# Kernel tuning notes

Hardware: AMD Instinct MI355X
Metric: run time of the kernel (lower is better)

## Reference

```python
import jax, jax.numpy as jnp
import numpy as np

DIM_V = 1024
NUM_HEADS = 64            # per the module arg name; actually the per-chunk size
DIM_SPLIT = DIM_V // NUM_HEADS  # 16 = effective number of attention heads (module quirk)
N_Q, N_K = 2048, 2048
DIM_Q, DIM_K = 1024, 1024


def setup_inputs() -> dict:
    key = jax.random.key(0)
    ks = jax.random.split(key, 10)
    s = 0.02
    return {
        "Q": jax.random.normal(ks[0], (N_Q, DIM_Q), dtype=jnp.float32),
        "K": jax.random.normal(ks[1], (N_K, DIM_K), dtype=jnp.float32),
        "Wq": jax.random.normal(ks[2], (DIM_V, DIM_Q), dtype=jnp.float32) * s,
        "bq": jax.random.normal(ks[3], (DIM_V,), dtype=jnp.float32) * s,
        "Wk": jax.random.normal(ks[4], (DIM_V, DIM_K), dtype=jnp.float32) * s,
        "bk": jax.random.normal(ks[5], (DIM_V,), dtype=jnp.float32) * s,
        "Wv": jax.random.normal(ks[6], (DIM_V, DIM_K), dtype=jnp.float32) * s,
        "bv": jax.random.normal(ks[7], (DIM_V,), dtype=jnp.float32) * s,
        "Wo": jax.random.normal(ks[8], (DIM_V, DIM_V), dtype=jnp.float32) * s,
        "bo": jax.random.normal(ks[9], (DIM_V,), dtype=jnp.float32) * s,
    }


def _split_heads(x):
    # jnp.split(x[None], DIM_SPLIT, axis=2) then concat on axis 0 ==
    # [DIM_SPLIT, n, NUM_HEADS] with chunk h = x[:, h*NUM_HEADS:(h+1)*NUM_HEADS]
    n = x.shape[0]
    return x.reshape(n, DIM_SPLIT, NUM_HEADS).transpose(1, 0, 2)


def reference(Q, K, Wq, bq, Wk, bk, Wv, bv, Wo, bo):
    q = Q @ Wq.T + bq            # [n_q, dim_V]
    k = K @ Wk.T + bk            # [n_k, dim_V]
    v = K @ Wv.T + bv            # [n_k, dim_V]
    Q_ = _split_heads(q)         # [H, n_q, d] with H=DIM_SPLIT, d=NUM_HEADS
    K_ = _split_heads(k)
    V_ = _split_heads(v)
    # Faithful to source: softmax first, THEN divide by sqrt(dim_V)
    A = jax.nn.softmax(jnp.einsum('hqd,hkd->hqk', Q_, K_), axis=-1)
    A = A / jnp.sqrt(jnp.float32(DIM_V))
    O = (Q_ + jnp.einsum('hqk,hkd->hqd', A, V_)).reshape(-1, DIM_V)  # [n_q, dim_V]
    # res1 = identity (ln=False)
    O = O + jax.nn.relu(O @ Wo.T + bo)
    # res2 = identity (ln=False)
    return O
```

## Files before the change

kernel.cpp:

```cpp
#include <hip/hip_runtime.h>
#include <cstdint>

typedef unsigned short u16;
typedef __attribute__((ext_vector_type(8))) short short8;
typedef __attribute__((ext_vector_type(4))) float f32x4;

__device__ __forceinline__ u16 f2b(float f) {
  uint32_t u = __float_as_uint(f);
  u += 0x7fffu + ((u >> 16) & 1u);
  return (u16)(u >> 16);
}
__device__ __forceinline__ float b2f(u16 b) {
  return __uint_as_float(((uint32_t)b) << 16);
}

__global__ __launch_bounds__(256) void cast_all(
    const float* __restrict__ Q, const float* __restrict__ K,
    const float* __restrict__ Wq, const float* __restrict__ Wk,
    const float* __restrict__ Wv, const float* __restrict__ Wo,
    u16* __restrict__ xq, u16* __restrict__ xk,
    u16* __restrict__ wq, u16* __restrict__ wk,
    u16* __restrict__ wv, u16* __restrict__ wo) {
  int g = blockIdx.x * 256 + threadIdx.x;
  const float* src; u16* dst; int off;
  if      (g <  524288) { src = Q;  dst = xq; off = g; }
  else if (g < 1048576) { src = K;  dst = xk; off = g -  524288; }
  else if (g < 1310720) { src = Wq; dst = wq; off = g - 1048576; }
  else if (g < 1572864) { src = Wk; dst = wk; off = g - 1310720; }
  else if (g < 1835008) { src = Wv; dst = wv; off = g - 1572864; }
  else                  { src = Wo; dst = wo; off = g - 1835008; }
  float4 v = reinterpret_cast<const float4*>(src)[off];
  ushort4 o4;
  o4.x = f2b(v.x); o4.y = f2b(v.y); o4.z = f2b(v.z); o4.w = f2b(v.w);
  reinterpret_cast<ushort4*>(dst)[off] = o4;
}

__global__ __launch_bounds__(256) void gemm3(
    const u16* __restrict__ xq, const u16* __restrict__ xk,
    const u16* __restrict__ wq, const u16* __restrict__ wk,
    const u16* __restrict__ wv,
    const float* __restrict__ bq, const float* __restrict__ bk,
    const float* __restrict__ bv,
    u16* __restrict__ qb, u16* __restrict__ kb, u16* __restrict__ vT) {
  __shared__ __align__(16) u16 sA[64 * 40];
  __shared__ __align__(16) u16 sB[64 * 40];
  const int t = threadIdx.x, blk = blockIdx.x, z = blockIdx.y;
  const u16 *A, *B; const float* bias; u16* C; int ldC, mbase, nbase; bool brow;
  if (z == 0)      { A = xq; B = wq; bias = bq; C = qb; ldC = 1024;
                     mbase = (blk >> 4) * 64; nbase = (blk & 15) * 64; brow = false; }
  else if (z == 1) { A = xk; B = wk; bias = bk; C = kb; ldC = 1024;
                     mbase = (blk >> 4) * 64; nbase = (blk & 15) * 64; brow = false; }
  else             { A = wv; B = xk; bias = bv; C = vT; ldC = 2048;
                     mbase = (blk >> 5) * 64; nbase = (blk & 31) * 64; brow = true; }
  const int lane = t & 63, wid = t >> 6;
  const int wy = wid >> 1, wx = wid & 1;
  const int m = lane & 15, quad = lane >> 4;
  const int srow = t >> 2, scb = (t & 3) * 8;
  const u16* gA = A + (mbase + srow) * 1024 + scb;
  const u16* gB = B + (nbase + srow) * 1024 + scb;
  uint4 ra = *(const uint4*)gA;
  uint4 rb = *(const uint4*)gB;

  f32x4 acc[2][2];
#pragma unroll
  for (int i = 0; i < 2; i++)
#pragma unroll
    for (int j = 0; j < 2; j++) acc[i][j] = (f32x4){0.f, 0.f, 0.f, 0.f};

  for (int kb_ = 0; kb_ < 32; ++kb_) {
    __syncthreads();
    *(uint4*)(&sA[srow * 40 + scb]) = ra;
    *(uint4*)(&sB[srow * 40 + scb]) = rb;
    if (kb_ < 31) {
      ra = *(const uint4*)(gA + (kb_ + 1) * 32);
      rb = *(const uint4*)(gB + (kb_ + 1) * 32);
    }
    __syncthreads();
    short8 af[2], bf[2];
#pragma unroll
    for (int mi = 0; mi < 2; mi++)
      af[mi] = *(const short8*)(&sA[(wy * 32 + mi * 16 + m) * 40 + quad * 8]);
#pragma unroll
    for (int ni = 0; ni < 2; ni++)
      bf[ni] = *(const short8*)(&sB[(wx * 32 + ni * 16 + m) * 40 + quad * 8]);
#pragma unroll
    for (int mi = 0; mi < 2; mi++)
#pragma unroll
      for (int ni = 0; ni < 2; ni++)
        acc[mi][ni] = __builtin_amdgcn_mfma_f32_16x16x32_bf16(
            af[mi], bf[ni], acc[mi][ni], 0, 0, 0);
  }

#pragma unroll
  for (int mi = 0; mi < 2; mi++)
#pragma unroll
    for (int ni = 0; ni < 2; ni++) {
      const int col = nbase + wx * 32 + ni * 16 + m;
      const float bcol = brow ? 0.f : bias[col];
#pragma unroll
      for (int r = 0; r < 4; r++) {
        const int row = mbase + wy * 32 + mi * 16 + quad * 4 + r;
        const float bval = brow ? bias[row] : bcol;
        C[row * ldC + col] = f2b(acc[mi][ni][r] + bval);
      }
    }
}

__global__ __launch_bounds__(256) void gemm_out(
    const u16* __restrict__ A, const u16* __restrict__ B,
    const float* __restrict__ bias, const u16* __restrict__ Res,
    float* __restrict__ out) {
  __shared__ __align__(16) u16 sA[64 * 40];
  __shared__ __align__(16) u16 sB[64 * 40];
  const int t = threadIdx.x, blk = blockIdx.x;
  const int mbase = (blk >> 4) * 64, nbase = (blk & 15) * 64;
  const int lane = t & 63, wid = t >> 6;
  const int wy = wid >> 1, wx = wid & 1;
  const int m = lane & 15, quad = lane >> 4;
  const int srow = t >> 2, scb = (t & 3) * 8;
  const u16* gA = A + (mbase + srow) * 1024 + scb;
  const u16* gB = B + (nbase + srow) * 1024 + scb;
  uint4 ra = *(const uint4*)gA;
  uint4 rb = *(const uint4*)gB;

  f32x4 acc[2][2];
#pragma unroll
  for (int i = 0; i < 2; i++)
#pragma unroll
    for (int j = 0; j < 2; j++) acc[i][j] = (f32x4){0.f, 0.f, 0.f, 0.f};

  for (int kb_ = 0; kb_ < 32; ++kb_) {
    __syncthreads();
    *(uint4*)(&sA[srow * 40 + scb]) = ra;
    *(uint4*)(&sB[srow * 40 + scb]) = rb;
    if (kb_ < 31) {
      ra = *(const uint4*)(gA + (kb_ + 1) * 32);
      rb = *(const uint4*)(gB + (kb_ + 1) * 32);
    }
    __syncthreads();
    short8 af[2], bf[2];
#pragma unroll
    for (int mi = 0; mi < 2; mi++)
      af[mi] = *(const short8*)(&sA[(wy * 32 + mi * 16 + m) * 40 + quad * 8]);
#pragma unroll
    for (int ni = 0; ni < 2; ni++)
      bf[ni] = *(const short8*)(&sB[(wx * 32 + ni * 16 + m) * 40 + quad * 8]);
#pragma unroll
    for (int mi = 0; mi < 2; mi++)
#pragma unroll
      for (int ni = 0; ni < 2; ni++)
        acc[mi][ni] = __builtin_amdgcn_mfma_f32_16x16x32_bf16(
            af[mi], bf[ni], acc[mi][ni], 0, 0, 0);
  }

#pragma unroll
  for (int mi = 0; mi < 2; mi++)
#pragma unroll
    for (int ni = 0; ni < 2; ni++) {
      const int col = nbase + wx * 32 + ni * 16 + m;
      const float bcol = bias[col];
#pragma unroll
      for (int r = 0; r < 4; r++) {
        const int row = mbase + wy * 32 + mi * 16 + quad * 4 + r;
        out[row * 1024 + col] =
            b2f(Res[row * 1024 + col]) + fmaxf(acc[mi][ni][r] + bcol, 0.f);
      }
    }
}

__global__ __launch_bounds__(256) void flash(
    const u16* __restrict__ q, const u16* __restrict__ k,
    const u16* __restrict__ vT, u16* __restrict__ po, float* __restrict__ lp) {
  __shared__ __align__(16) u16 sK[64 * 72];
  __shared__ __align__(16) u16 sV[64 * 72];
  __shared__ __align__(16) u16 sP[4 * 32 * 72];
  const int t = threadIdx.x;
  const int qt = blockIdx.x, h = blockIdx.y, sp = blockIdx.z;
  const int lane = t & 63, wid = t >> 6;
  const int m = lane & 15, quad = lane >> 4;
  const int colbase = h * 64;
  const int pbase = wid * 2304;
  const int kbase = sp * 1024;

  short8 aq[2][2];
#pragma unroll
  for (int mi = 0; mi < 2; mi++)
#pragma unroll
    for (int g = 0; g < 2; g++)
      aq[mi][g] = *(const short8*)(
          &q[(qt * 128 + wid * 32 + mi * 16 + m) * 1024 + colbase + g * 32 + quad * 8]);

  f32x4 o[2][4];
  float lpart[2][4];
#pragma unroll
  for (int mi = 0; mi < 2; mi++)
#pragma unroll
    for (int nt = 0; nt < 4; nt++) o[mi][nt] = (f32x4){0.f, 0.f, 0.f, 0.f};
#pragma unroll
  for (int mi = 0; mi < 2; mi++)
#pragma unroll
    for (int r = 0; r < 4; r++) lpart[mi][r] = 0.f;

  const int srow = t >> 2, scb = (t & 3) * 16;
  const u16* gK = k + (kbase + srow) * 1024 + colbase + scb;
  const u16* gV = vT + (colbase + srow) * 2048 + kbase + scb;

  uint4 rk0 = *(const uint4*)(gK), rk1 = *(const uint4*)(gK + 8);
  uint4 rv0 = *(const uint4*)(gV), rv1 = *(const uint4*)(gV + 8);

  for (int kt = 0; kt < 16; ++kt) {
    __syncthreads();
    *(uint4*)(&sK[srow * 72 + scb])     = rk0;
    *(uint4*)(&sK[srow * 72 + scb + 8]) = rk1;
    *(uint4*)(&sV[srow * 72 + scb])     = rv0;
    *(uint4*)(&sV[srow * 72 + scb + 8]) = rv1;
    if (kt < 15) {
      rk0 = *(const uint4*)(gK + (kt + 1) * 65536);
      rk1 = *(const uint4*)(gK + (kt + 1) * 65536 + 8);
      rv0 = *(const uint4*)(gV + (kt + 1) * 64);
      rv1 = *(const uint4*)(gV + (kt + 1) * 64 + 8);
    }
    __syncthreads();

    f32x4 s[2][4];
#pragma unroll
    for (int nt = 0; nt < 4; nt++) {
      short8 bk0 = *(const short8*)(&sK[(nt * 16 + m) * 72 + quad * 8]);
      short8 bk1 = *(const short8*)(&sK[(nt * 16 + m) * 72 + 32 + quad * 8]);
#pragma unroll
      for (int mi = 0; mi < 2; mi++) {
        f32x4 a = (f32x4){0.f, 0.f, 0.f, 0.f};
        a = __builtin_amdgcn_mfma_f32_16x16x32_bf16(aq[mi][0], bk0, a, 0, 0, 0);
        a = __builtin_amdgcn_mfma_f32_16x16x32_bf16(aq[mi][1], bk1, a, 0, 0, 0);
        s[mi][nt] = a;
      }
    }

#pragma unroll
    for (int mi = 0; mi < 2; mi++)
#pragma unroll
      for (int nt = 0; nt < 4; nt++)
#pragma unroll
        for (int r = 0; r < 4; r++) {
          const float p = __expf(s[mi][nt][r] - 16.0f);
          lpart[mi][r] += p;
          sP[pbase + (mi * 16 + quad * 4 + r) * 72 + nt * 16 + m] = f2b(p);
        }

    short8 pa[2][2];
#pragma unroll
    for (int mi = 0; mi < 2; mi++)
#pragma unroll
      for (int g = 0; g < 2; g++)
        pa[mi][g] = *(const short8*)(&sP[pbase + (mi * 16 + m) * 72 + g * 32 + quad * 8]);
#pragma unroll
    for (int nt = 0; nt < 4; nt++) {
      short8 bv0 = *(const short8*)(&sV[(nt * 16 + m) * 72 + quad * 8]);
      short8 bv1 = *(const short8*)(&sV[(nt * 16 + m) * 72 + 32 + quad * 8]);
#pragma unroll
      for (int mi = 0; mi < 2; mi++) {
        o[mi][nt] = __builtin_amdgcn_mfma_f32_16x16x32_bf16(pa[mi][0], bv0, o[mi][nt], 0, 0, 0);
        o[mi][nt] = __builtin_amdgcn_mfma_f32_16x16x32_bf16(pa[mi][1], bv1, o[mi][nt], 0, 0, 0);
      }
    }
  }

#pragma unroll
  for (int mi = 0; mi < 2; mi++)
#pragma unroll
    for (int r = 0; r < 4; r++) {
#pragma unroll
      for (int off = 1; off < 16; off <<= 1)
        lpart[mi][r] += __shfl_xor(lpart[mi][r], off);
    }

#pragma unroll
  for (int mi = 0; mi < 2; mi++)
#pragma unroll
    for (int r = 0; r < 4; r++) {
      const int qg = qt * 128 + wid * 32 + mi * 16 + quad * 4 + r;
      const int base = ((sp * 16 + h) * 2048 + qg) * 64;
#pragma unroll
      for (int nt = 0; nt < 4; nt++)
        po[base + nt * 16 + m] = f2b(o[mi][nt][r]);
      if (m == 0) lp[(sp * 16 + h) * 2048 + qg] = lpart[mi][r];
    }
}

__global__ __launch_bounds__(256) void combine(
    const u16* __restrict__ po, const float* __restrict__ lp,
    const u16* __restrict__ qb, u16* __restrict__ ob) {
  const int idx = blockIdx.x * 256 + threadIdx.x;
  const int dq = idx & 15, qg = (idx >> 4) & 2047, h = idx >> 15;
  float acc0 = 0.f, acc1 = 0.f, acc2 = 0.f, acc3 = 0.f, l = 0.f;
#pragma unroll
  for (int s = 0; s < 2; s++) {
    const ushort4 p4 = *(const ushort4*)&po[(((s * 16 + h) * 2048 + qg) * 64) + dq * 4];
    acc0 += b2f(p4.x); acc1 += b2f(p4.y); acc2 += b2f(p4.z); acc3 += b2f(p4.w);
    l += lp[(s * 16 + h) * 2048 + qg];
  }
  const float inv = 1.0f / (l * 32.0f);
  const ushort4 q4 = *(const ushort4*)&qb[qg * 1024 + h * 64 + dq * 4];
  ushort4 o4;
  o4.x = f2b(b2f(q4.x) + acc0 * inv);
  o4.y = f2b(b2f(q4.y) + acc1 * inv);
  o4.z = f2b(b2f(q4.z) + acc2 * inv);
  o4.w = f2b(b2f(q4.w) + acc3 * inv);
  *(ushort4*)&ob[(h * 128 + (qg >> 4)) * 1024 + (qg & 15) * 64 + dq * 4] = o4;
}

extern "C" void kernel_launch(void* const* d_in, const int* in_sizes, int n_in,
                              void* d_out, int out_size, void* d_ws, size_t ws_size,
                              hipStream_t stream) {
  const float* Q  = (const float*)d_in[0];
  const float* K  = (const float*)d_in[1];
  const float* Wq = (const float*)d_in[2];
  const float* bq = (const float*)d_in[3];
  const float* Wk = (const float*)d_in[4];
  const float* bk = (const float*)d_in[5];
  const float* Wv = (const float*)d_in[6];
  const float* bv = (const float*)d_in[7];
  const float* Wo = (const float*)d_in[8];
  const float* bo = (const float*)d_in[9];
  float* out = (float*)d_out;

  u16* ws = (u16*)d_ws;
  u16* xq  = ws;
  u16* xk  = xq  + 2097152;
  u16* wqb = xk  + 2097152;
  u16* wkb = wqb + 1048576;
  u16* wvb = wkb + 1048576;
  u16* wob = wvb + 1048576;
  u16* qb  = wob + 1048576;
  u16* kb  = qb  + 2097152;
  u16* vT  = kb  + 2097152;
  u16* ob  = vT  + 2097152;
  u16*   po = ws;
  float* lp = (float*)(ws + 4194304);

  cast_all<<<8192, 256, 0, stream>>>(Q, K, Wq, Wk, Wv, Wo, xq, xk, wqb, wkb, wvb, wob);

  gemm3<<<dim3(512, 3), 256, 0, stream>>>(xq, xk, wqb, wkb, wvb, bq, bk, bv, qb, kb, vT);

  flash<<<dim3(16, 16, 2), 256, 0, stream>>>(qb, kb, vT, po, lp);

  combine<<<2048, 256, 0, stream>>>(po, lp, qb, ob);

  gemm_out<<<512, 256, 0, stream>>>(ob, wob, bo, ob, out);
}
```

Measured before the change: 176.7 us.

## Enlarge gemm3 M tile, split flash keys 4-way, transpose QK^T MFMA for packed P stores

The projection GEMM now uses 128x64 tiles with four M fragments per wave, which halves the block count and raises B-tile reuse. The flash kernel splits the key range into four chunks instead of two, giving more blocks for parallelism. It also swaps the MFMA operands so each lane holds a row of S, which lets P be stored as packed bf16 pairs and shortens the row-sum reduction to two shuffles. The combine kernel now reads four partials, and the partial buffers move to a separate workspace region, at the cost of more partial-output traffic.

```diff
diff --git a/kernel.cpp b/kernel.cpp
--- a/kernel.cpp
+++ b/kernel.cpp
@@ -1,4 +1,5 @@
 #include <hip/hip_runtime.h>
+#include <hip/hip_bf16.h>
 #include <cstdint>
 
 typedef unsigned short u16;
@@ -12,6 +13,10 @@
 }
 __device__ __forceinline__ float b2f(u16 b) {
   return __uint_as_float(((uint32_t)b) << 16);
+}
+__device__ __forceinline__ uint32_t pk2bf(float a, float b) {
+  __hip_bfloat162 t = __float22bfloat162_rn(make_float2(a, b));
+  return *(uint32_t*)&t;
 }
 
 __global__ __launch_bounds__(256) void cast_all(
@@ -42,49 +47,55 @@
     const float* __restrict__ bq, const float* __restrict__ bk,
     const float* __restrict__ bv,
     u16* __restrict__ qb, u16* __restrict__ kb, u16* __restrict__ vT) {
-  __shared__ __align__(16) u16 sA[64 * 40];
+  __shared__ __align__(16) u16 sA[128 * 40];
   __shared__ __align__(16) u16 sB[64 * 40];
   const int t = threadIdx.x, blk = blockIdx.x, z = blockIdx.y;
   const u16 *A, *B; const float* bias; u16* C; int ldC, mbase, nbase; bool brow;
   if (z == 0)      { A = xq; B = wq; bias = bq; C = qb; ldC = 1024;
-                     mbase = (blk >> 4) * 64; nbase = (blk & 15) * 64; brow = false; }
+                     mbase = (blk >> 4) * 128; nbase = (blk & 15) * 64; brow = false; }
   else if (z == 1) { A = xk; B = wk; bias = bk; C = kb; ldC = 1024;
-                     mbase = (blk >> 4) * 64; nbase = (blk & 15) * 64; brow = false; }
+                     mbase = (blk >> 4) * 128; nbase = (blk & 15) * 64; brow = false; }
   else             { A = wv; B = xk; bias = bv; C = vT; ldC = 2048;
-                     mbase = (blk >> 5) * 64; nbase = (blk & 31) * 64; brow = true; }
+                     mbase = (blk >> 5) * 128; nbase = (blk & 31) * 64; brow = true; }
   const int lane = t & 63, wid = t >> 6;
   const int wy = wid >> 1, wx = wid & 1;
   const int m = lane & 15, quad = lane >> 4;
-  const int srow = t >> 2, scb = (t & 3) * 8;
-  const u16* gA = A + (mbase + srow) * 1024 + scb;
-  const u16* gB = B + (nbase + srow) * 1024 + scb;
-  uint4 ra = *(const uint4*)gA;
-  uint4 rb = *(const uint4*)gB;
-
-  f32x4 acc[2][2];
-#pragma unroll
-  for (int i = 0; i < 2; i++)
+
+  const int arow = t >> 1, acb = (t & 1) * 16;
+  const int brow_ = t >> 2, bcb = (t & 3) * 8;
+  const u16* gA = A + (mbase + arow) * 1024 + acb;
+  const u16* gB = B + (nbase + brow_) * 1024 + bcb;
+
+  uint4 ra0 = *(const uint4*)(gA);
+  uint4 ra1 = *(const uint4*)(gA + 8);
+  uint4 rb0 = *(const uint4*)(gB);
+
+  f32x4 acc[4][2];
+#pragma unroll
+  for (int i = 0; i < 4; i++)
 #pragma unroll
     for (int j = 0; j < 2; j++) acc[i][j] = (f32x4){0.f, 0.f, 0.f, 0.f};
 
   for (int kb_ = 0; kb_ < 32; ++kb_) {
     __syncthreads();
-    *(uint4*)(&sA[srow * 40 + scb]) = ra;
-    *(uint4*)(&sB[srow * 40 + scb]) = rb;
+    *(uint4*)(&sA[arow * 40 + acb])     = ra0;
+    *(uint4*)(&sA[arow * 40 + acb + 8]) = ra1;
+    *(uint4*)(&sB[brow_ * 40 + bcb])    = rb0;
     if (kb_ < 31) {
-      ra = *(const uint4*)(gA + (kb_ + 1) * 32);
-      rb = *(const uint4*)(gB + (kb_ + 1) * 32);
-    }
-    __syncthreads();
-    short8 af[2], bf[2];
-#pragma unroll
-    for (int mi = 0; mi < 2; mi++)
-      af[mi] = *(const short8*)(&sA[(wy * 32 + mi * 16 + m) * 40 + quad * 8]);
+      ra0 = *(const uint4*)(gA + (kb_ + 1) * 32);
+      ra1 = *(const uint4*)(gA + (kb_ + 1) * 32 + 8);
+      rb0 = *(const uint4*)(gB + (kb_ + 1) * 32);
+    }
+    __syncthreads();
+    short8 af[4], bf[2];
+#pragma unroll
+    for (int mi = 0; mi < 4; mi++)
+      af[mi] = *(const short8*)(&sA[(wy * 64 + mi * 16 + m) * 40 + quad * 8]);
 #pragma unroll
     for (int ni = 0; ni < 2; ni++)
       bf[ni] = *(const short8*)(&sB[(wx * 32 + ni * 16 + m) * 40 + quad * 8]);
 #pragma unroll
-    for (int mi = 0; mi < 2; mi++)
+    for (int mi = 0; mi < 4; mi++)
 #pragma unroll
       for (int ni = 0; ni < 2; ni++)
         acc[mi][ni] = __builtin_amdgcn_mfma_f32_16x16x32_bf16(
@@ -92,14 +103,14 @@
   }
 
 #pragma unroll
-  for (int mi = 0; mi < 2; mi++)
+  for (int mi = 0; mi < 4; mi++)
 #pragma unroll
     for (int ni = 0; ni < 2; ni++) {
       const int col = nbase + wx * 32 + ni * 16 + m;
       const float bcol = brow ? 0.f : bias[col];
 #pragma unroll
       for (int r = 0; r < 4; r++) {
-        const int row = mbase + wy * 32 + mi * 16 + quad * 4 + r;
+        const int row = mbase + wy * 64 + mi * 16 + quad * 4 + r;
         const float bval = brow ? bias[row] : bcol;
         C[row * ldC + col] = f2b(acc[mi][ni][r] + bval);
       }
@@ -180,7 +191,7 @@
   const int m = lane & 15, quad = lane >> 4;
   const int colbase = h * 64;
   const int pbase = wid * 2304;
-  const int kbase = sp * 1024;
+  const int kbase = sp * 512;
 
   short8 aq[2][2];
 #pragma unroll
@@ -191,15 +202,11 @@
           &q[(qt * 128 + wid * 32 + mi * 16 + m) * 1024 + colbase + g * 32 + quad * 8]);
 
   f32x4 o[2][4];
-  float lpart[2][4];
+  float lpart[2] = {0.f, 0.f};
 #pragma unroll
   for (int mi = 0; mi < 2; mi++)
 #pragma unroll
     for (int nt = 0; nt < 4; nt++) o[mi][nt] = (f32x4){0.f, 0.f, 0.f, 0.f};
-#pragma unroll
-  for (int mi = 0; mi < 2; mi++)
-#pragma unroll
-    for (int r = 0; r < 4; r++) lpart[mi][r] = 0.f;
 
   const int srow = t >> 2, scb = (t & 3) * 16;
   const u16* gK = k + (kbase + srow) * 1024 + colbase + scb;
@@ -208,13 +215,15 @@
   uint4 rk0 = *(const uint4*)(gK), rk1 = *(const uint4*)(gK + 8);
   uint4 rv0 = *(const uint4*)(gV), rv1 = *(const uint4*)(gV + 8);
 
-  for (int kt = 0; kt < 16; ++kt) {
+  uint32_t* sP32 = (uint32_t*)sP;
+
+  for (int kt = 0; kt < 8; ++kt) {
     __syncthreads();
     *(uint4*)(&sK[srow * 72 + scb])     = rk0;
     *(uint4*)(&sK[srow * 72 + scb + 8]) = rk1;
     *(uint4*)(&sV[srow * 72 + scb])     = rv0;
     *(uint4*)(&sV[srow * 72 + scb + 8]) = rv1;
-    if (kt < 15) {
+    if (kt < 7) {
       rk0 = *(const uint4*)(gK + (kt + 1) * 65536);
       rk1 = *(const uint4*)(gK + (kt + 1) * 65536 + 8);
       rv0 = *(const uint4*)(gV + (kt + 1) * 64);
@@ -222,30 +231,25 @@
     }
     __syncthreads();
 
-    f32x4 s[2][4];
 #pragma unroll
     for (int nt = 0; nt < 4; nt++) {
       short8 bk0 = *(const short8*)(&sK[(nt * 16 + m) * 72 + quad * 8]);
       short8 bk1 = *(const short8*)(&sK[(nt * 16 + m) * 72 + 32 + quad * 8]);
 #pragma unroll
       for (int mi = 0; mi < 2; mi++) {
-        f32x4 a = (f32x4){0.f, 0.f, 0.f, 0.f};
-        a = __builtin_amdgcn_mfma_f32_16x16x32_bf16(aq[mi][0], bk0, a, 0, 0, 0);
-        a = __builtin_amdgcn_mfma_f32_16x16x32_bf16(aq[mi][1], bk1, a, 0, 0, 0);
-        s[mi][nt] = a;
+        f32x4 st = (f32x4){0.f, 0.f, 0.f, 0.f};
+        st = __builtin_amdgcn_mfma_f32_16x16x32_bf16(bk0, aq[mi][0], st, 0, 0, 0);
+        st = __builtin_amdgcn_mfma_f32_16x16x32_bf16(bk1, aq[mi][1], st, 0, 0, 0);
+        float p0 = __expf(st[0] - 16.0f);
+        float p1 = __expf(st[1] - 16.0f);
+        float p2 = __expf(st[2] - 16.0f);
+        float p3 = __expf(st[3] - 16.0f);
+        lpart[mi] += (p0 + p1) + (p2 + p3);
+        const int pa_ = pbase + (mi * 16 + m) * 72 + nt * 16 + quad * 4;
+        sP32[pa_ >> 1]       = pk2bf(p0, p1);
+        sP32[(pa_ >> 1) + 1] = pk2bf(p2, p3);
       }
     }
-
-#pragma unroll
-    for (int mi = 0; mi < 2; mi++)
-#pragma unroll
-      for (int nt = 0; nt < 4; nt++)
-#pragma unroll
-        for (int r = 0; r < 4; r++) {
-          const float p = __expf(s[mi][nt][r] - 16.0f);
-          lpart[mi][r] += p;
-          sP[pbase + (mi * 16 + quad * 4 + r) * 72 + nt * 16 + m] = f2b(p);
-        }
 
     short8 pa[2][2];
 #pragma unroll
@@ -266,13 +270,13 @@
   }
 
 #pragma unroll
-  for (int mi = 0; mi < 2; mi++)
-#pragma unroll
-    for (int r = 0; r < 4; r++) {
-#pragma unroll
-      for (int off = 1; off < 16; off <<= 1)
-        lpart[mi][r] += __shfl_xor(lpart[mi][r], off);
-    }
+  for (int mi = 0; mi < 2; mi++) {
+    float l = lpart[mi];
+    l += __shfl_xor(l, 16);
+    l += __shfl_xor(l, 32);
+    if (quad == 0)
+      lp[(sp * 16 + h) * 2048 + qt * 128 + wid * 32 + mi * 16 + m] = l;
+  }
 
 #pragma unroll
   for (int mi = 0; mi < 2; mi++)
@@ -283,7 +287,6 @@
 #pragma unroll
       for (int nt = 0; nt < 4; nt++)
         po[base + nt * 16 + m] = f2b(o[mi][nt][r]);
-      if (m == 0) lp[(sp * 16 + h) * 2048 + qg] = lpart[mi][r];
     }
 }
 
@@ -294,7 +297,7 @@
   const int dq = idx & 15, qg = (idx >> 4) & 2047, h = idx >> 15;
   float acc0 = 0.f, acc1 = 0.f, acc2 = 0.f, acc3 = 0.f, l = 0.f;
 #pragma unroll
-  for (int s = 0; s < 2; s++) {
+  for (int s = 0; s < 4; s++) {
     const ushort4 p4 = *(const ushort4*)&po[(((s * 16 + h) * 2048 + qg) * 64) + dq * 4];
     acc0 += b2f(p4.x); acc1 += b2f(p4.y); acc2 += b2f(p4.z); acc3 += b2f(p4.w);
     l += lp[(s * 16 + h) * 2048 + qg];
@@ -335,14 +338,14 @@
   u16* kb  = qb  + 2097152;
   u16* vT  = kb  + 2097152;
   u16* ob  = vT  + 2097152;
-  u16*   po = ws;
-  float* lp = (float*)(ws + 4194304);
+  u16* po  = ob  + 2097152;
+  float* lp = (float*)(po + 8388608);
 
   cast_all<<<8192, 256, 0, stream>>>(Q, K, Wq, Wk, Wv, Wo, xq, xk, wqb, wkb, wvb, wob);
 
-  gemm3<<<dim3(512, 3), 256, 0, stream>>>(xq, xk, wqb, wkb, wvb, bq, bk, bv, qb, kb, vT);
-
-  flash<<<dim3(16, 16, 2), 256, 0, stream>>>(qb, kb, vT, po, lp);
+  gemm3<<<dim3(256, 3), 256, 0, stream>>>(xq, xk, wqb, wkb, wvb, bq, bk, bv, qb, kb, vT);
+
+  flash<<<dim3(16, 16, 4), 256, 0, stream>>>(qb, kb, vT, po, lp);
 
   combine<<<2048, 256, 0, stream>>>(po, lp, qb, ob);
 
```

After: 172.8 us. 2.2% less time.
